# Kernel optimization log

Hardware: AMD Instinct MI355X
Metric: run time of the kernel (lower is better)

The kernel has to match this reference:

```python
import jax, jax.numpy as jnp
import numpy as np

N, E, H, C, F_IN = 10000, 160000, 8, 128, 4  # nodes, edges, heads, per-head dim, input feats
D = H * C  # 1024 concat dim


def _gelu(v):
    return jax.nn.gelu(v, approximate=False)  # torch F.gelu default is exact erf


def _gat(x, src, dst, w, a_s, a_d, b):
    """PyG GATConv (concat=True, negative_slope=0.2), self-loops already in src/dst."""
    n = x.shape[0]
    h = (x @ w).reshape(n, H, C)                      # [N,H,C]
    e = (h * a_s).sum(-1)[src] + (h * a_d).sum(-1)[dst]  # [E,H] per-edge logits
    e = jnp.where(e > 0, e, 0.2 * e)                  # LeakyReLU(0.2)
    m = jax.lax.stop_gradient(jax.ops.segment_max(e, dst, num_segments=n))
    p = jnp.exp(e - m[dst])
    z = jax.ops.segment_sum(p, dst, num_segments=n)   # [N,H]
    alpha = p / z[dst]                                # softmax over incoming edges
    out = jax.ops.segment_sum(h[src] * alpha[:, :, None], dst, num_segments=n)
    return out.reshape(n, D) + b


def setup_inputs() -> dict:
    key = jax.random.key(0)
    ks = jax.random.split(key, 24)
    s = 0.05
    inp = {
        "x": jax.random.normal(ks[0], (N, F_IN), dtype=jnp.float32),
        "edge_index": jax.random.randint(ks[1], (2, E), 0, N),
        "w1": jax.random.normal(ks[2], (F_IN, D)) * s,
        "asrc1": jax.random.normal(ks[3], (H, C)) * s,
        "adst1": jax.random.normal(ks[4], (H, C)) * s,
        "bias1": jnp.zeros((D,), jnp.float32),
        "w2": jax.random.normal(ks[5], (C, D)) * s,
        "asrc2": jax.random.normal(ks[6], (H, C)) * s,
        "adst2": jax.random.normal(ks[7], (H, C)) * s,
        "bias2": jnp.zeros((D,), jnp.float32),
        "w3": jax.random.normal(ks[8], (C, D)) * s,
        "asrc3": jax.random.normal(ks[9], (H, C)) * s,
        "adst3": jax.random.normal(ks[10], (H, C)) * s,
        "bias3": jnp.zeros((D,), jnp.float32),
        "rw1": jax.random.normal(ks[11], (D, C)) * s,
        "rb1": jnp.zeros((C,), jnp.float32),
        "rw2": jax.random.normal(ks[12], (D, C)) * s,
        "rb2": jnp.zeros((C,), jnp.float32),
        "lw": jax.random.normal(ks[13], (D, C)) * s,
        "lb": jnp.zeros((C,), jnp.float32),
    }
    return inp


def reference(x, edge_index, w1, asrc1, adst1, bias1, w2, asrc2, adst2, bias2,
              w3, asrc3, adst3, bias3, rw1, rb1, rw2, rb2, lw, lb):
    loops = jnp.arange(N, dtype=edge_index.dtype)
    src = jnp.concatenate([edge_index[0], loops])
    dst = jnp.concatenate([edge_index[1], loops])
    h = _gat(x, src, dst, w1, asrc1, adst1, bias1)            # [N, 1024]
    h = _gat(_gelu(h) @ rw1 + rb1, src, dst, w2, asrc2, adst2, bias2)
    h = _gat(_gelu(h) @ rw2 + rb2, src, dst, w3, asrc3, adst3, bias3)
    return _gelu(h) @ lw + lb                                 # [N, 128]
```

## Files before the change

### kernel.cpp

```cpp
#include <hip/hip_runtime.h>
#include <hip/hip_fp16.h>
#include <math.h>


#define THREADS 256
#define CAP 128

typedef _Float16 f16x8 __attribute__((ext_vector_type(8)));
typedef float f32x4 __attribute__((ext_vector_type(4)));

struct __align__(8) Half4 { __half2 a, b; };

__device__ __forceinline__ float gelu_exact(float x) {
  return 0.5f * x * (1.0f + erff(x * 0.70710678118654752f));
}


__global__ __launch_bounds__(256) void prep_kernel(
    const int* __restrict__ ei, int E, int ET, int* __restrict__ counts,
    const float* __restrict__ w2, const float* __restrict__ w3,
    const float* __restrict__ rw1, const float* __restrict__ rw2,
    const float* __restrict__ lw,
    __half* __restrict__ wt2, __half* __restrict__ wt3,
    __half* __restrict__ rwt1, __half* __restrict__ rwt2,
    __half* __restrict__ lwt,
    const float* __restrict__ w1,
    const float* __restrict__ as1, const float* __restrict__ ad1,
    const float* __restrict__ as2, const float* __restrict__ ad2,
    const float* __restrict__ as3, const float* __restrict__ ad3,
    float* __restrict__ ws1, float* __restrict__ wd1,
    float* __restrict__ ws2, float* __restrict__ wd2,
    float* __restrict__ ws3, float* __restrict__ wd3,
    int nHist) {
  __shared__ float tile[32][33];
  int bid = blockIdx.x;
  int t = threadIdx.x;

  if (bid < nHist) {
    int e = bid * 256 + t;
    if (e >= ET) return;
    int d = (e < E) ? ei[E + e] : (e - E);
    atomicAdd(&counts[d], 1);
    return;
  }
  bid -= nHist;
  if (bid < 640) {
    const float* in; __half* out; int K, Ncol;
    int z = bid >> 7, rem = bid & 127;
    switch (z) {
      case 0: in = w2;  out = wt2;  K = 128;  Ncol = 1024; break;
      case 1: in = w3;  out = wt3;  K = 128;  Ncol = 1024; break;
      case 2: in = rw1; out = rwt1; K = 1024; Ncol = 128;  break;
      case 3: in = rw2; out = rwt2; K = 1024; Ncol = 128;  break;
      default: in = lw; out = lwt;  K = 1024; Ncol = 128;  break;
    }
    int kt, ct;
    if (z < 2) { kt = rem >> 5; ct = rem & 31; }
    else       { kt = rem & 31; ct = rem >> 5; }
    int kb = kt * 32, cb = ct * 32;
    int tc = t & 31, tr = t >> 5;
#pragma unroll
    for (int r = tr; r < 32; r += 8)
      tile[r][tc] = in[(size_t)(kb + r) * Ncol + cb + tc];
    __syncthreads();
#pragma unroll
    for (int r = tr; r < 32; r += 8)
      out[(size_t)(cb + r) * K + kb + tc] = __float2half_rn(tile[tc][r]);
    return;
  }
  bid -= 640;
  {
    int h = bid & 7, yy = bid >> 3;
    int sel = t >> 7;
    int k = t & 127;
    const float* W; const float* av; float* outp; int K;
    switch (yy) {
      case 0: W = w2; av = sel ? ad2 : as2; outp = sel ? wd2 : ws2; K = 128; break;
      case 1: W = w3; av = sel ? ad3 : as3; outp = sel ? wd3 : ws3; K = 128; break;
      default: W = w1; av = sel ? ad1 : as1; outp = sel ? wd1 : ws1; K = 4; break;
    }
    if (k >= K) return;
    const float* wrow = W + (size_t)k * 1024 + h * 128;
    const float* arow = av + h * 128;
    float s = 0.f;
    for (int c = 0; c < 128; c += 4) {
      float4 wv = *(const float4*)&wrow[c];
      float4 a4 = *(const float4*)&arow[c];
      s += wv.x * a4.x + wv.y * a4.y + wv.z * a4.z + wv.w * a4.w;
    }
    outp[h * K + k] = s;
  }
}


__global__ __launch_bounds__(1024) void scan_scores_kernel(
    const int* __restrict__ counts, int* __restrict__ offsets,
    int* __restrict__ cursor, int n,
    const float* __restrict__ x,
    const float* __restrict__ ws1, const float* __restrict__ wd1,
    float* __restrict__ ssrc, float* __restrict__ sdst, int total) {
  __shared__ int sums[1024];
  if (blockIdx.x == 0) {
    int t = threadIdx.x;
    int per = (n + 1023) >> 10;
    int start = t * per; if (start > n) start = n;
    int end = start + per; if (end > n) end = n;
    int local = 0;
    for (int i = start; i < end; ++i) local += counts[i];
    sums[t] = local;
    __syncthreads();
    for (int off = 1; off < 1024; off <<= 1) {
      int add = (t >= off) ? sums[t - off] : 0;
      __syncthreads();
      sums[t] += add;
      __syncthreads();
    }
    int run = (t == 0) ? 0 : sums[t - 1];
    for (int i = start; i < end; ++i) {
      offsets[i] = run; cursor[i] = run; run += counts[i];
    }
    if (t == 1023) offsets[n] = run;
    return;
  }
  int idx = (blockIdx.x - 1) * 1024 + threadIdx.x;
  if (idx >= total) return;
  int nn = idx >> 3, h = idx & 7;
  float4 xv = *(const float4*)&x[nn * 4];
  float4 a = *(const float4*)&ws1[h * 4];
  float4 b = *(const float4*)&wd1[h * 4];
  ssrc[idx] = xv.x * a.x + xv.y * a.y + xv.z * a.z + xv.w * a.w;
  sdst[idx] = xv.x * b.x + xv.y * b.y + xv.z * b.z + xv.w * b.w;
}

__global__ void scatter_kernel(const int* __restrict__ ei, int E, int ET,
                               int* __restrict__ cursor, int* __restrict__ srcs) {
  int e = blockIdx.x * THREADS + threadIdx.x;
  if (e >= ET) return;
  int s = (e < E) ? ei[e] : (e - E);
  int d = (e < E) ? ei[E + e] : (e - E);
  int pos = atomicAdd(&cursor[d], 1);
  srcs[pos] = s;
}


__global__ __launch_bounds__(256) void attnagg_p(const __half* __restrict__ P16,
                                                 const int* __restrict__ srcs,
                                                 const int* __restrict__ offsets,
                                                 const float* __restrict__ ssrc,
                                                 const float* __restrict__ sdst,
                                                 __half* __restrict__ Y16, int NP) {
  __shared__ float lal[4][CAP][8];
  __shared__ int ls[4][CAP];
  __shared__ float szinv[4][8];
  int w = threadIdx.x >> 6, lane = threadIdx.x & 63;
  int n = blockIdx.x * 4 + w;
  int start = offsets[n], deg = offsets[n + 1] - start;
  int head = lane & 7, es = lane >> 3;
  float sd = sdst[n * 8 + head];
  int c2 = lane * 2;
  float accx[8] = {}, accy[8] = {};
  float s = 0.f;
  for (int cc = 0; cc < deg; cc += CAP) {
    int cm = min(CAP, deg - cc);
    for (int i = es; i < cm; i += 8) {
      int sp = srcs[start + cc + i];
      float v = ssrc[sp * 8 + head] + sd;
      v = (v > 0.f) ? v : 0.2f * v;
      float e = __expf(v);
      lal[w][i][head] = e;
      if (head == 0) ls[w][i] = sp;
      s += e;
    }
    int i = 0;
    for (; i + 1 < cm; i += 2) {
      int sp0 = ls[w][i], sp1 = ls[w][i + 1];
      float4 a00 = *(float4*)&lal[w][i][0];
      float4 a01 = *(float4*)&lal[w][i][4];
      float4 a10 = *(float4*)&lal[w][i + 1][0];
      float4 a11 = *(float4*)&lal[w][i + 1][4];
      float2 p0 = __half22float2(*(const __half2*)&P16[(size_t)sp0 * 128 + c2]);
      float2 p1 = __half22float2(*(const __half2*)&P16[(size_t)sp1 * 128 + c2]);
      float a0[8] = {a00.x, a00.y, a00.z, a00.w, a01.x, a01.y, a01.z, a01.w};
      float a1[8] = {a10.x, a10.y, a10.z, a10.w, a11.x, a11.y, a11.z, a11.w};
#pragma unroll
      for (int h = 0; h < 8; ++h) {
        accx[h] += a0[h] * p0.x; accy[h] += a0[h] * p0.y;
        accx[h] += a1[h] * p1.x; accy[h] += a1[h] * p1.y;
      }
    }
    if (i < cm) {
      int sp0 = ls[w][i];
      float4 a00 = *(float4*)&lal[w][i][0];
      float4 a01 = *(float4*)&lal[w][i][4];
      float2 p0 = __half22float2(*(const __half2*)&P16[(size_t)sp0 * 128 + c2]);
      float a0[8] = {a00.x, a00.y, a00.z, a00.w, a01.x, a01.y, a01.z, a01.w};
#pragma unroll
      for (int h = 0; h < 8; ++h) {
        accx[h] += a0[h] * p0.x; accy[h] += a0[h] * p0.y;
      }
    }
  }
#pragma unroll
  for (int mask = 8; mask <= 32; mask <<= 1)
    s += __shfl_xor(s, mask);
  if (es == 0) szinv[w][head] = 1.f / s;
#pragma unroll
  for (int h = 0; h < 8; ++h) {
    float zi = szinv[w][h];
    *(__half2*)&Y16[((size_t)h * NP + n) * 128 + c2] =
        __floats2half2_rn(accx[h] * zi, accy[h] * zi);
  }
}


__global__ __launch_bounds__(256) void attnagg_x(const float* __restrict__ x,
                                                 const int* __restrict__ srcs,
                                                 const int* __restrict__ offsets,
                                                 const float* __restrict__ ssrc,
                                                 const float* __restrict__ sdst,
                                                 float* __restrict__ Y1, int NP) {
  __shared__ float lal[4][CAP][8];
  __shared__ int ls[4][CAP];
  __shared__ float szinv[4][8];
  int w = threadIdx.x >> 6, lane = threadIdx.x & 63;
  int n = blockIdx.x * 4 + w;
  int start = offsets[n], deg = offsets[n + 1] - start;
  int head = lane & 7, es = lane >> 3;
  float sd = sdst[n * 8 + head];
  int eo = lane >> 5, hb = (lane >> 2) & 7, ch = lane & 3;
  float acc = 0.f;
  float s = 0.f;
  for (int cc = 0; cc < deg; cc += CAP) {
    int cm = min(CAP, deg - cc);
    for (int i = es; i < cm; i += 8) {
      int sp = srcs[start + cc + i];
      float v = ssrc[sp * 8 + head] + sd;
      v = (v > 0.f) ? v : 0.2f * v;
      float e = __expf(v);
      lal[w][i][head] = e;
      if (head == 0) ls[w][i] = sp;
      s += e;
    }
    for (int i = eo; i < cm; i += 2) {
      int sp = ls[w][i];
      float a = lal[w][i][hb];
      acc += a * x[sp * 4 + ch];
    }
  }
#pragma unroll
  for (int mask = 8; mask <= 32; mask <<= 1)
    s += __shfl_xor(s, mask);
  if (es == 0) szinv[w][head] = 1.f / s;
  acc += __shfl_xor(acc, 32);
  if (lane < 32) {
    float zi = szinv[w][hb];
    Y1[((size_t)hb * NP + n) * 4 + ch] = acc * zi;
  }
}


template <typename OutT, bool SC>
__global__ __launch_bounds__(512) void tail_mfma(const __half* __restrict__ Y16,
                                                 const __half* __restrict__ WtA,
                                                 const float* __restrict__ biasA,
                                                 const __half* __restrict__ WtP,
                                                 const float* __restrict__ biasP,
                                                 OutT* __restrict__ out, int N, int NP,
                                                 const float* __restrict__ wsn,
                                                 const float* __restrict__ wdn,
                                                 float* __restrict__ ssrc,
                                                 float* __restrict__ sdst) {
  __shared__ __half Gt[32][1032];
  __shared__ __half Pl[32][136];
  int w = threadIdx.x >> 6, lane = threadIdx.x & 63;
  int r0 = blockIdx.x * 32;
  int m = lane & 15, quad = lane >> 4;
  {
    int h = w;
    const __half* py0 = Y16 + ((size_t)h * NP + r0 + m) * 128 + quad * 8;
    const __half* py1 = py0 + (size_t)16 * 128;
    f16x8 bf0[4], bf1[4];
#pragma unroll
    for (int kk = 0; kk < 4; ++kk) {
      bf0[kk] = *(const f16x8*)(py0 + kk * 32);
      bf1[kk] = *(const f16x8*)(py1 + kk * 32);
    }
#pragma unroll
    for (int tile = 0; tile < 8; ++tile) {
      int gc = h * 128 + tile * 16;
      const __half* pa = WtA + (size_t)(gc + m) * 128 + quad * 8;
      f16x8 a[4];
#pragma unroll
      for (int kk = 0; kk < 4; ++kk) a[kk] = *(const f16x8*)(pa + kk * 32);
      f32x4 acc0 = {0.f, 0.f, 0.f, 0.f}, acc1 = {0.f, 0.f, 0.f, 0.f};
#pragma unroll
      for (int kk = 0; kk < 4; ++kk) {
        acc0 = __builtin_amdgcn_mfma_f32_16x16x32_f16(a[kk], bf0[kk], acc0, 0, 0, 0);
        acc1 = __builtin_amdgcn_mfma_f32_16x16x32_f16(a[kk], bf1[kk], acc1, 0, 0, 0);
      }
      float4 b4 = *(const float4*)&biasA[gc + quad * 4];
      Half4 p0, p1;
      p0.a = __floats2half2_rn(gelu_exact(acc0[0] + b4.x), gelu_exact(acc0[1] + b4.y));
      p0.b = __floats2half2_rn(gelu_exact(acc0[2] + b4.z), gelu_exact(acc0[3] + b4.w));
      p1.a = __floats2half2_rn(gelu_exact(acc1[0] + b4.x), gelu_exact(acc1[1] + b4.y));
      p1.b = __floats2half2_rn(gelu_exact(acc1[2] + b4.z), gelu_exact(acc1[3] + b4.w));
      *(Half4*)&Gt[m][gc + quad * 4] = p0;
      *(Half4*)&Gt[16 + m][gc + quad * 4] = p1;
    }
  }
  __syncthreads();
  {
    int c0 = w * 16;
    const __half* pa = WtP + (size_t)(c0 + m) * 1024 + quad * 8;
    f32x4 acc0 = {0.f, 0.f, 0.f, 0.f}, acc1 = {0.f, 0.f, 0.f, 0.f};
#pragma unroll 8
    for (int k = 0; k < 1024; k += 32) {
      f16x8 a = *(const f16x8*)(pa + k);
      f16x8 b0 = *(const f16x8*)&Gt[m][quad * 8 + k];
      f16x8 b1 = *(const f16x8*)&Gt[16 + m][quad * 8 + k];
      acc0 = __builtin_amdgcn_mfma_f32_16x16x32_f16(a, b0, acc0, 0, 0, 0);
      acc1 = __builtin_amdgcn_mfma_f32_16x16x32_f16(a, b1, acc1, 0, 0, 0);
    }
    float4 b4 = *(const float4*)&biasP[c0 + quad * 4];
    int row0 = r0 + m, row1 = r0 + 16 + m;
    if constexpr (__is_same(OutT, __half)) {
      Half4 p, q;
      p.a = __floats2half2_rn(acc0[0] + b4.x, acc0[1] + b4.y);
      p.b = __floats2half2_rn(acc0[2] + b4.z, acc0[3] + b4.w);
      q.a = __floats2half2_rn(acc1[0] + b4.x, acc1[1] + b4.y);
      q.b = __floats2half2_rn(acc1[2] + b4.z, acc1[3] + b4.w);
      if constexpr (SC) {
        *(Half4*)&Pl[m][c0 + quad * 4] = p;
        *(Half4*)&Pl[16 + m][c0 + quad * 4] = q;
      }
      if (row0 < N) *(Half4*)&out[(size_t)row0 * 128 + c0 + quad * 4] = p;
      if (row1 < N) *(Half4*)&out[(size_t)row1 * 128 + c0 + quad * 4] = q;
    } else {
      if (row0 < N)
        *(float4*)&out[(size_t)row0 * 128 + c0 + quad * 4] =
            make_float4(acc0[0] + b4.x, acc0[1] + b4.y, acc0[2] + b4.z, acc0[3] + b4.w);
      if (row1 < N)
        *(float4*)&out[(size_t)row1 * 128 + c0 + quad * 4] =
            make_float4(acc1[0] + b4.x, acc1[1] + b4.y, acc1[2] + b4.z, acc1[3] + b4.w);
    }
  }
  if constexpr (SC) {
    __syncthreads();
    int head = lane & 7, es = lane >> 3;
    const float* wsp = wsn + head * 128 + es * 16;
    const float* wdp = wdn + head * 128 + es * 16;
    float wsr[16], wdr[16];
#pragma unroll
    for (int j = 0; j < 16; ++j) { wsr[j] = wsp[j]; wdr[j] = wdp[j]; }
#pragma unroll
    for (int r = 0; r < 4; ++r) {
      int row = w * 4 + r;
      f16x8 p0 = *(const f16x8*)&Pl[row][es * 16];
      f16x8 p1 = *(const f16x8*)&Pl[row][es * 16 + 8];
      float s1 = 0.f, s2 = 0.f;
#pragma unroll
      for (int j = 0; j < 8; ++j) {
        float v = (float)p0[j];
        s1 += v * wsr[j]; s2 += v * wdr[j];
      }
#pragma unroll
      for (int j = 0; j < 8; ++j) {
        float v = (float)p1[j];
        s1 += v * wsr[8 + j]; s2 += v * wdr[8 + j];
      }
#pragma unroll
      for (int mask = 8; mask <= 32; mask <<= 1) {
        s1 += __shfl_xor(s1, mask);
        s2 += __shfl_xor(s2, mask);
      }
      int nn = r0 + row;
      if (es == 0 && nn < N) { ssrc[nn * 8 + head] = s1; sdst[nn * 8 + head] = s2; }
    }
  }
}


template <typename OutT, bool SC>
__global__ __launch_bounds__(512) void tail1_kernel(const float* __restrict__ Y1,
                                                    const float* __restrict__ w,
                                                    const float* __restrict__ biasA,
                                                    const __half* __restrict__ WtP,
                                                    const float* __restrict__ biasP,
                                                    OutT* __restrict__ out, int N, int NP,
                                                    const float* __restrict__ wsn,
                                                    const float* __restrict__ wdn,
                                                    float* __restrict__ ssrc,
                                                    float* __restrict__ sdst) {
  __shared__ __half Gt[32][1032];
  __shared__ __half Pl[32][136];
  int t = threadIdx.x;
  int r0 = blockIdx.x * 32;
  {
    int c0 = (t & 255) * 4;
    int h = c0 >> 7;
    float4 wa = *(const float4*)&w[c0];
    float4 wb = *(const float4*)&w[1024 + c0];
    float4 wc = *(const float4*)&w[2048 + c0];
    float4 wd = *(const float4*)&w[3072 + c0];
    float4 b4 = *(const float4*)&biasA[c0];
#pragma unroll 4
    for (int r = t >> 8; r < 32; r += 2) {
      float4 yv = *(const float4*)&Y1[((size_t)h * NP + r0 + r) * 4];
      float o0 = gelu_exact(yv.x * wa.x + yv.y * wb.x + yv.z * wc.x + yv.w * wd.x + b4.x);
      float o1 = gelu_exact(yv.x * wa.y + yv.y * wb.y + yv.z * wc.y + yv.w * wd.y + b4.y);
      float o2 = gelu_exact(yv.x * wa.z + yv.y * wb.z + yv.z * wc.z + yv.w * wd.z + b4.z);
      float o3 = gelu_exact(yv.x * wa.w + yv.y * wb.w + yv.z * wc.w + yv.w * wd.w + b4.w);
      Half4 p;
      p.a = __floats2half2_rn(o0, o1);
      p.b = __floats2half2_rn(o2, o3);
      *(Half4*)&Gt[r][c0] = p;
    }
  }
  __syncthreads();
  int wv = t >> 6, lane = t & 63;
  int m = lane & 15, quad = lane >> 4;
  {
    int c0 = wv * 16;
    const __half* pa = WtP + (size_t)(c0 + m) * 1024 + quad * 8;
    f32x4 acc0 = {0.f, 0.f, 0.f, 0.f}, acc1 = {0.f, 0.f, 0.f, 0.f};
#pragma unroll 8
    for (int k = 0; k < 1024; k += 32) {
      f16x8 a = *(const f16x8*)(pa + k);
      f16x8 b0 = *(const f16x8*)&Gt[m][quad * 8 + k];
      f16x8 b1 = *(const f16x8*)&Gt[16 + m][quad * 8 + k];
      acc0 = __builtin_amdgcn_mfma_f32_16x16x32_f16(a, b0, acc0, 0, 0, 0);
      acc1 = __builtin_amdgcn_mfma_f32_16x16x32_f16(a, b1, acc1, 0, 0, 0);
    }
    float4 b4 = *(const float4*)&biasP[c0 + quad * 4];
    int row0 = r0 + m, row1 = r0 + 16 + m;
    if constexpr (__is_same(OutT, __half)) {
      Half4 p, q;
      p.a = __floats2half2_rn(acc0[0] + b4.x, acc0[1] + b4.y);
      p.b = __floats2half2_rn(acc0[2] + b4.z, acc0[3] + b4.w);
      q.a = __floats2half2_rn(acc1[0] + b4.x, acc1[1] + b4.y);
      q.b = __floats2half2_rn(acc1[2] + b4.z, acc1[3] + b4.w);
      if constexpr (SC) {
        *(Half4*)&Pl[m][c0 + quad * 4] = p;
        *(Half4*)&Pl[16 + m][c0 + quad * 4] = q;
      }
      if (row0 < N) *(Half4*)&out[(size_t)row0 * 128 + c0 + quad * 4] = p;
      if (row1 < N) *(Half4*)&out[(size_t)row1 * 128 + c0 + quad * 4] = q;
    } else {
      if (row0 < N)
        *(float4*)&out[(size_t)row0 * 128 + c0 + quad * 4] =
            make_float4(acc0[0] + b4.x, acc0[1] + b4.y, acc0[2] + b4.z, acc0[3] + b4.w);
      if (row1 < N)
        *(float4*)&out[(size_t)row1 * 128 + c0 + quad * 4] =
            make_float4(acc1[0] + b4.x, acc1[1] + b4.y, acc1[2] + b4.z, acc1[3] + b4.w);
    }
  }
  if constexpr (SC) {
    __syncthreads();
    int head = lane & 7, es = lane >> 3;
    const float* wsp = wsn + head * 128 + es * 16;
    const float* wdp = wdn + head * 128 + es * 16;
    float wsr[16], wdr[16];
#pragma unroll
    for (int j = 0; j < 16; ++j) { wsr[j] = wsp[j]; wdr[j] = wdp[j]; }
#pragma unroll
    for (int r = 0; r < 4; ++r) {
      int row = wv * 4 + r;
      f16x8 p0 = *(const f16x8*)&Pl[row][es * 16];
      f16x8 p1 = *(const f16x8*)&Pl[row][es * 16 + 8];
      float s1 = 0.f, s2 = 0.f;
#pragma unroll
      for (int j = 0; j < 8; ++j) {
        float v = (float)p0[j];
        s1 += v * wsr[j]; s2 += v * wdr[j];
      }
#pragma unroll
      for (int j = 0; j < 8; ++j) {
        float v = (float)p1[j];
        s1 += v * wsr[8 + j]; s2 += v * wdr[8 + j];
      }
#pragma unroll
      for (int mask = 8; mask <= 32; mask <<= 1) {
        s1 += __shfl_xor(s1, mask);
        s2 += __shfl_xor(s2, mask);
      }
      int nn = r0 + row;
      if (es == 0 && nn < N) { ssrc[nn * 8 + head] = s1; sdst[nn * 8 + head] = s2; }
    }
  }
}


extern "C" void kernel_launch(void* const* d_in, const int* in_sizes, int n_in,
                              void* d_out, int out_size, void* d_ws, size_t ws_size,
                              hipStream_t stream) {
  const float* x   = (const float*)d_in[0];
  const int*   ei  = (const int*)d_in[1];
  const float* w1  = (const float*)d_in[2];
  const float* as1 = (const float*)d_in[3];
  const float* ad1 = (const float*)d_in[4];
  const float* b1  = (const float*)d_in[5];
  const float* w2  = (const float*)d_in[6];
  const float* as2 = (const float*)d_in[7];
  const float* ad2 = (const float*)d_in[8];
  const float* b2  = (const float*)d_in[9];
  const float* w3  = (const float*)d_in[10];
  const float* as3 = (const float*)d_in[11];
  const float* ad3 = (const float*)d_in[12];
  const float* b3  = (const float*)d_in[13];
  const float* rw1 = (const float*)d_in[14];
  const float* rb1 = (const float*)d_in[15];
  const float* rw2 = (const float*)d_in[16];
  const float* rb2 = (const float*)d_in[17];
  const float* lw  = (const float*)d_in[18];
  const float* lb  = (const float*)d_in[19];

  int N = in_sizes[0] / 4;
  int E = in_sizes[1] / 2;
  int ET = E + N;
  int nRow32 = (N + 31) / 32;
  int NP = nRow32 * 32;
  (void)ws_size;

  char* wsb = (char*)d_ws;
  size_t off = 0;
  auto alloc = [&](size_t bytes) -> void* {
    void* p = wsb + off;
    off += (bytes + 255) & ~(size_t)255;
    return p;
  };
  __half* P16  = (__half*)alloc((size_t)N * 128 * 2);
  __half* Y16  = (__half*)alloc((size_t)8 * NP * 128 * 2);
  float*  Y1   = (float*)alloc((size_t)8 * NP * 4 * 4);
  __half* wt2  = (__half*)alloc((size_t)1024 * 128 * 2);
  __half* wt3  = (__half*)alloc((size_t)1024 * 128 * 2);
  __half* rwt1 = (__half*)alloc((size_t)128 * 1024 * 2);
  __half* rwt2 = (__half*)alloc((size_t)128 * 1024 * 2);
  __half* lwt  = (__half*)alloc((size_t)128 * 1024 * 2);
  float* ws1 = (float*)alloc(8 * 4 * 4);
  float* wd1 = (float*)alloc(8 * 4 * 4);
  float* ws2 = (float*)alloc(8 * 128 * 4);
  float* wd2 = (float*)alloc(8 * 128 * 4);
  float* ws3 = (float*)alloc(8 * 128 * 4);
  float* wd3 = (float*)alloc(8 * 128 * 4);
  float* ssrc   = (float*)alloc((size_t)N * 8 * 4);
  float* sdst   = (float*)alloc((size_t)N * 8 * 4);
  int* counts  = (int*)alloc((size_t)N * 4);
  int* offsets = (int*)alloc((size_t)(N + 1) * 4);
  int* cursor  = (int*)alloc((size_t)N * 4);
  int* srcs    = (int*)alloc((size_t)ET * 4);

  dim3 blk(THREADS);
  dim3 blk512(512);

  int nHist = (ET + THREADS - 1) / THREADS;

  hipMemsetAsync(counts, 0, (size_t)N * 4, stream);

  prep_kernel<<<dim3(nHist + 640 + 24), blk, 0, stream>>>(
      ei, E, ET, counts,
      w2, w3, rw1, rw2, lw, wt2, wt3, rwt1, rwt2, lwt,
      w1, as1, ad1, as2, ad2, as3, ad3,
      ws1, wd1, ws2, wd2, ws3, wd3, nHist);

  int total1 = N * 8;
  int nSc = (total1 + 1023) / 1024;
  scan_scores_kernel<<<dim3(1 + nSc), dim3(1024), 0, stream>>>(
      counts, offsets, cursor, N, x, ws1, wd1, ssrc, sdst, total1);

  scatter_kernel<<<dim3(nHist), blk, 0, stream>>>(ei, E, ET, cursor, srcs);

  dim3 gNode4(N / 4);
  dim3 gRow32(nRow32);

  attnagg_x<<<gNode4, blk, 0, stream>>>(x, srcs, offsets, ssrc, sdst, Y1, NP);
  tail1_kernel<__half, true><<<gRow32, blk512, 0, stream>>>(
      Y1, w1, b1, rwt1, rb1, P16, N, NP, ws2, wd2, ssrc, sdst);

  attnagg_p<<<gNode4, blk, 0, stream>>>(P16, srcs, offsets, ssrc, sdst, Y16, NP);
  tail_mfma<__half, true><<<gRow32, blk512, 0, stream>>>(
      Y16, wt2, b2, rwt2, rb2, P16, N, NP, ws3, wd3, ssrc, sdst);

  attnagg_p<<<gNode4, blk, 0, stream>>>(P16, srcs, offsets, ssrc, sdst, Y16, NP);
  tail_mfma<float, false><<<gRow32, blk512, 0, stream>>>(
      Y16, wt3, b3, lwt, lb, (float*)d_out, N, NP, nullptr, nullptr, nullptr, nullptr);
}
```

Before: 287.9 us.

## Fuse attention aggregation into per-layer MFMA tail kernels via shared memory

Merges each layer's edge aggregation kernel into the following dense MFMA kernel. Each 512-thread block aggregates its 32 rows straight into LDS instead of writing the 8-head Y16/Y1 intermediates to global memory and reading them back. This drops three launches and the global round trip of the large intermediate. The node features and attention scores are now double-buffered so that a fused kernel never overwrites the buffers its neighbours still read. In exchange, there are fewer blocks (32 rows each instead of 4 nodes), the gather phase has less parallelism, and the larger LDS footprint may lower occupancy.

```diff
diff --git a/kernel.cpp b/kernel.cpp
--- a/kernel.cpp
+++ b/kernel.cpp
@@ -4,7 +4,6 @@
 
 
 #define THREADS 256
-#define CAP 128
 
 typedef _Float16 f16x8 __attribute__((ext_vector_type(8)));
 typedef float f32x4 __attribute__((ext_vector_type(4)));
@@ -143,259 +142,62 @@
 }
 
 
-__global__ __launch_bounds__(256) void attnagg_p(const __half* __restrict__ P16,
-                                                 const int* __restrict__ srcs,
-                                                 const int* __restrict__ offsets,
-                                                 const float* __restrict__ ssrc,
-                                                 const float* __restrict__ sdst,
-                                                 __half* __restrict__ Y16, int NP) {
-  __shared__ float lal[4][CAP][8];
-  __shared__ int ls[4][CAP];
-  __shared__ float szinv[4][8];
-  int w = threadIdx.x >> 6, lane = threadIdx.x & 63;
-  int n = blockIdx.x * 4 + w;
-  int start = offsets[n], deg = offsets[n + 1] - start;
+__global__ __launch_bounds__(512) void layer1_kernel(
+    const float* __restrict__ x,
+    const int* __restrict__ srcs, const int* __restrict__ offsets,
+    const float* __restrict__ ssrc, const float* __restrict__ sdst,
+    const float* __restrict__ w, const float* __restrict__ biasA,
+    const __half* __restrict__ WtP, const float* __restrict__ biasP,
+    __half* __restrict__ out, int N,
+    const float* __restrict__ wsn, const float* __restrict__ wdn,
+    float* __restrict__ ssrc_n, float* __restrict__ sdst_n) {
+  __shared__ __half Gt[32][1032];
+  __shared__ float Y1l[32][36];
+  __shared__ __align__(16) char scratch[9216];
+  __shared__ float szinv[8][8];
+  float (*lsc)[32][8] = reinterpret_cast<float(*)[32][8]>(scratch);
+  int (*lsi)[32] = reinterpret_cast<int(*)[32]>(scratch + 8192);
+  __half (*Pl)[136] = reinterpret_cast<__half(*)[136]>(scratch);
+
+  int wv = threadIdx.x >> 6, lane = threadIdx.x & 63;
+  int r0 = blockIdx.x * 32;
   int head = lane & 7, es = lane >> 3;
-  float sd = sdst[n * 8 + head];
-  int c2 = lane * 2;
-  float accx[8] = {}, accy[8] = {};
-  float s = 0.f;
-  for (int cc = 0; cc < deg; cc += CAP) {
-    int cm = min(CAP, deg - cc);
-    for (int i = es; i < cm; i += 8) {
-      int sp = srcs[start + cc + i];
-      float v = ssrc[sp * 8 + head] + sd;
-      v = (v > 0.f) ? v : 0.2f * v;
-      float e = __expf(v);
-      lal[w][i][head] = e;
-      if (head == 0) ls[w][i] = sp;
-      s += e;
-    }
-    int i = 0;
-    for (; i + 1 < cm; i += 2) {
-      int sp0 = ls[w][i], sp1 = ls[w][i + 1];
-      float4 a00 = *(float4*)&lal[w][i][0];
-      float4 a01 = *(float4*)&lal[w][i][4];
-      float4 a10 = *(float4*)&lal[w][i + 1][0];
-      float4 a11 = *(float4*)&lal[w][i + 1][4];
-      float2 p0 = __half22float2(*(const __half2*)&P16[(size_t)sp0 * 128 + c2]);
-      float2 p1 = __half22float2(*(const __half2*)&P16[(size_t)sp1 * 128 + c2]);
-      float a0[8] = {a00.x, a00.y, a00.z, a00.w, a01.x, a01.y, a01.z, a01.w};
-      float a1[8] = {a10.x, a10.y, a10.z, a10.w, a11.x, a11.y, a11.z, a11.w};
-#pragma unroll
-      for (int h = 0; h < 8; ++h) {
-        accx[h] += a0[h] * p0.x; accy[h] += a0[h] * p0.y;
-        accx[h] += a1[h] * p1.x; accy[h] += a1[h] * p1.y;
-      }
-    }
-    if (i < cm) {
-      int sp0 = ls[w][i];
-      float4 a00 = *(float4*)&lal[w][i][0];
-      float4 a01 = *(float4*)&lal[w][i][4];
-      float2 p0 = __half22float2(*(const __half2*)&P16[(size_t)sp0 * 128 + c2]);
-      float a0[8] = {a00.x, a00.y, a00.z, a00.w, a01.x, a01.y, a01.z, a01.w};
-#pragma unroll
-      for (int h = 0; h < 8; ++h) {
-        accx[h] += a0[h] * p0.x; accy[h] += a0[h] * p0.y;
-      }
-    }
-  }
-#pragma unroll
-  for (int mask = 8; mask <= 32; mask <<= 1)
-    s += __shfl_xor(s, mask);
-  if (es == 0) szinv[w][head] = 1.f / s;
-#pragma unroll
-  for (int h = 0; h < 8; ++h) {
-    float zi = szinv[w][h];
-    *(__half2*)&Y16[((size_t)h * NP + n) * 128 + c2] =
-        __floats2half2_rn(accx[h] * zi, accy[h] * zi);
-  }
-}
-
-
-__global__ __launch_bounds__(256) void attnagg_x(const float* __restrict__ x,
-                                                 const int* __restrict__ srcs,
-                                                 const int* __restrict__ offsets,
-                                                 const float* __restrict__ ssrc,
-                                                 const float* __restrict__ sdst,
-                                                 float* __restrict__ Y1, int NP) {
-  __shared__ float lal[4][CAP][8];
-  __shared__ int ls[4][CAP];
-  __shared__ float szinv[4][8];
-  int w = threadIdx.x >> 6, lane = threadIdx.x & 63;
-  int n = blockIdx.x * 4 + w;
-  int start = offsets[n], deg = offsets[n + 1] - start;
-  int head = lane & 7, es = lane >> 3;
-  float sd = sdst[n * 8 + head];
   int eo = lane >> 5, hb = (lane >> 2) & 7, ch = lane & 3;
-  float acc = 0.f;
-  float s = 0.f;
-  for (int cc = 0; cc < deg; cc += CAP) {
-    int cm = min(CAP, deg - cc);
-    for (int i = es; i < cm; i += 8) {
-      int sp = srcs[start + cc + i];
-      float v = ssrc[sp * 8 + head] + sd;
-      v = (v > 0.f) ? v : 0.2f * v;
-      float e = __expf(v);
-      lal[w][i][head] = e;
-      if (head == 0) ls[w][i] = sp;
-      s += e;
-    }
-    for (int i = eo; i < cm; i += 2) {
-      int sp = ls[w][i];
-      float a = lal[w][i][hb];
-      acc += a * x[sp * 4 + ch];
-    }
-  }
-#pragma unroll
-  for (int mask = 8; mask <= 32; mask <<= 1)
-    s += __shfl_xor(s, mask);
-  if (es == 0) szinv[w][head] = 1.f / s;
-  acc += __shfl_xor(acc, 32);
-  if (lane < 32) {
-    float zi = szinv[w][hb];
-    Y1[((size_t)hb * NP + n) * 4 + ch] = acc * zi;
-  }
-}
-
-
-template <typename OutT, bool SC>
-__global__ __launch_bounds__(512) void tail_mfma(const __half* __restrict__ Y16,
-                                                 const __half* __restrict__ WtA,
-                                                 const float* __restrict__ biasA,
-                                                 const __half* __restrict__ WtP,
-                                                 const float* __restrict__ biasP,
-                                                 OutT* __restrict__ out, int N, int NP,
-                                                 const float* __restrict__ wsn,
-                                                 const float* __restrict__ wdn,
-                                                 float* __restrict__ ssrc,
-                                                 float* __restrict__ sdst) {
-  __shared__ __half Gt[32][1032];
-  __shared__ __half Pl[32][136];
-  int w = threadIdx.x >> 6, lane = threadIdx.x & 63;
-  int r0 = blockIdx.x * 32;
-  int m = lane & 15, quad = lane >> 4;
-  {
-    int h = w;
-    const __half* py0 = Y16 + ((size_t)h * NP + r0 + m) * 128 + quad * 8;
-    const __half* py1 = py0 + (size_t)16 * 128;
-    f16x8 bf0[4], bf1[4];
-#pragma unroll
-    for (int kk = 0; kk < 4; ++kk) {
-      bf0[kk] = *(const f16x8*)(py0 + kk * 32);
-      bf1[kk] = *(const f16x8*)(py1 + kk * 32);
-    }
-#pragma unroll
-    for (int tile = 0; tile < 8; ++tile) {
-      int gc = h * 128 + tile * 16;
-      const __half* pa = WtA + (size_t)(gc + m) * 128 + quad * 8;
-      f16x8 a[4];
-#pragma unroll
-      for (int kk = 0; kk < 4; ++kk) a[kk] = *(const f16x8*)(pa + kk * 32);
-      f32x4 acc0 = {0.f, 0.f, 0.f, 0.f}, acc1 = {0.f, 0.f, 0.f, 0.f};
-#pragma unroll
-      for (int kk = 0; kk < 4; ++kk) {
-        acc0 = __builtin_amdgcn_mfma_f32_16x16x32_f16(a[kk], bf0[kk], acc0, 0, 0, 0);
-        acc1 = __builtin_amdgcn_mfma_f32_16x16x32_f16(a[kk], bf1[kk], acc1, 0, 0, 0);
-      }
-      float4 b4 = *(const float4*)&biasA[gc + quad * 4];
-      Half4 p0, p1;
-      p0.a = __floats2half2_rn(gelu_exact(acc0[0] + b4.x), gelu_exact(acc0[1] + b4.y));
-      p0.b = __floats2half2_rn(gelu_exact(acc0[2] + b4.z), gelu_exact(acc0[3] + b4.w));
-      p1.a = __floats2half2_rn(gelu_exact(acc1[0] + b4.x), gelu_exact(acc1[1] + b4.y));
-      p1.b = __floats2half2_rn(gelu_exact(acc1[2] + b4.z), gelu_exact(acc1[3] + b4.w));
-      *(Half4*)&Gt[m][gc + quad * 4] = p0;
-      *(Half4*)&Gt[16 + m][gc + quad * 4] = p1;
-    }
+
+  for (int j = 0; j < 4; ++j) {
+    int row = wv * 4 + j, n = r0 + row;
+    if (n >= N) {
+      if (lane < 32) Y1l[row][hb * 4 + ch] = 0.f;
+      continue;
+    }
+    int start = offsets[n], deg = offsets[n + 1] - start;
+    float sd = sdst[n * 8 + head];
+    float acc = 0.f, s = 0.f;
+    for (int cc = 0; cc < deg; cc += 32) {
+      int cm = min(32, deg - cc);
+      for (int i = es; i < cm; i += 8) {
+        int sp = srcs[start + cc + i];
+        float v = ssrc[sp * 8 + head] + sd;
+        v = (v > 0.f) ? v : 0.2f * v;
+        float e = __expf(v);
+        lsc[wv][i][head] = e;
+        if (head == 0) lsi[wv][i] = sp;
+        s += e;
+      }
+      for (int i = eo; i < cm; i += 2) {
+        int sp = lsi[wv][i];
+        acc += lsc[wv][i][hb] * x[sp * 4 + ch];
+      }
+    }
+#pragma unroll
+    for (int mask = 8; mask <= 32; mask <<= 1) s += __shfl_xor(s, mask);
+    if (es == 0) szinv[wv][head] = 1.f / s;
+    acc += __shfl_xor(acc, 32);
+    if (lane < 32) Y1l[row][hb * 4 + ch] = acc * szinv[wv][hb];
   }
   __syncthreads();
   {
-    int c0 = w * 16;
-    const __half* pa = WtP + (size_t)(c0 + m) * 1024 + quad * 8;
-    f32x4 acc0 = {0.f, 0.f, 0.f, 0.f}, acc1 = {0.f, 0.f, 0.f, 0.f};
-#pragma unroll 8
-    for (int k = 0; k < 1024; k += 32) {
-      f16x8 a = *(const f16x8*)(pa + k);
-      f16x8 b0 = *(const f16x8*)&Gt[m][quad * 8 + k];
-      f16x8 b1 = *(const f16x8*)&Gt[16 + m][quad * 8 + k];
-      acc0 = __builtin_amdgcn_mfma_f32_16x16x32_f16(a, b0, acc0, 0, 0, 0);
-      acc1 = __builtin_amdgcn_mfma_f32_16x16x32_f16(a, b1, acc1, 0, 0, 0);
-    }
-    float4 b4 = *(const float4*)&biasP[c0 + quad * 4];
-    int row0 = r0 + m, row1 = r0 + 16 + m;
-    if constexpr (__is_same(OutT, __half)) {
-      Half4 p, q;
-      p.a = __floats2half2_rn(acc0[0] + b4.x, acc0[1] + b4.y);
-      p.b = __floats2half2_rn(acc0[2] + b4.z, acc0[3] + b4.w);
-      q.a = __floats2half2_rn(acc1[0] + b4.x, acc1[1] + b4.y);
-      q.b = __floats2half2_rn(acc1[2] + b4.z, acc1[3] + b4.w);
-      if constexpr (SC) {
-        *(Half4*)&Pl[m][c0 + quad * 4] = p;
-        *(Half4*)&Pl[16 + m][c0 + quad * 4] = q;
-      }
-      if (row0 < N) *(Half4*)&out[(size_t)row0 * 128 + c0 + quad * 4] = p;
-      if (row1 < N) *(Half4*)&out[(size_t)row1 * 128 + c0 + quad * 4] = q;
-    } else {
-      if (row0 < N)
-        *(float4*)&out[(size_t)row0 * 128 + c0 + quad * 4] =
-            make_float4(acc0[0] + b4.x, acc0[1] + b4.y, acc0[2] + b4.z, acc0[3] + b4.w);
-      if (row1 < N)
-        *(float4*)&out[(size_t)row1 * 128 + c0 + quad * 4] =
-            make_float4(acc1[0] + b4.x, acc1[1] + b4.y, acc1[2] + b4.z, acc1[3] + b4.w);
-    }
-  }
-  if constexpr (SC) {
-    __syncthreads();
-    int head = lane & 7, es = lane >> 3;
-    const float* wsp = wsn + head * 128 + es * 16;
-    const float* wdp = wdn + head * 128 + es * 16;
-    float wsr[16], wdr[16];
-#pragma unroll
-    for (int j = 0; j < 16; ++j) { wsr[j] = wsp[j]; wdr[j] = wdp[j]; }
-#pragma unroll
-    for (int r = 0; r < 4; ++r) {
-      int row = w * 4 + r;
-      f16x8 p0 = *(const f16x8*)&Pl[row][es * 16];
-      f16x8 p1 = *(const f16x8*)&Pl[row][es * 16 + 8];
-      float s1 = 0.f, s2 = 0.f;
-#pragma unroll
-      for (int j = 0; j < 8; ++j) {
-        float v = (float)p0[j];
-        s1 += v * wsr[j]; s2 += v * wdr[j];
-      }
-#pragma unroll
-      for (int j = 0; j < 8; ++j) {
-        float v = (float)p1[j];
-        s1 += v * wsr[8 + j]; s2 += v * wdr[8 + j];
-      }
-#pragma unroll
-      for (int mask = 8; mask <= 32; mask <<= 1) {
-        s1 += __shfl_xor(s1, mask);
-        s2 += __shfl_xor(s2, mask);
-      }
-      int nn = r0 + row;
-      if (es == 0 && nn < N) { ssrc[nn * 8 + head] = s1; sdst[nn * 8 + head] = s2; }
-    }
-  }
-}
-
-
-template <typename OutT, bool SC>
-__global__ __launch_bounds__(512) void tail1_kernel(const float* __restrict__ Y1,
-                                                    const float* __restrict__ w,
-                                                    const float* __restrict__ biasA,
-                                                    const __half* __restrict__ WtP,
-                                                    const float* __restrict__ biasP,
-                                                    OutT* __restrict__ out, int N, int NP,
-                                                    const float* __restrict__ wsn,
-                                                    const float* __restrict__ wdn,
-                                                    float* __restrict__ ssrc,
-                                                    float* __restrict__ sdst) {
-  __shared__ __half Gt[32][1032];
-  __shared__ __half Pl[32][136];
-  int t = threadIdx.x;
-  int r0 = blockIdx.x * 32;
-  {
+    int t = threadIdx.x;
     int c0 = (t & 255) * 4;
     int h = c0 >> 7;
     float4 wa = *(const float4*)&w[c0];
@@ -405,7 +207,7 @@
     float4 b4 = *(const float4*)&biasA[c0];
 #pragma unroll 4
     for (int r = t >> 8; r < 32; r += 2) {
-      float4 yv = *(const float4*)&Y1[((size_t)h * NP + r0 + r) * 4];
+      float4 yv = *(const float4*)&Y1l[r][h * 4];
       float o0 = gelu_exact(yv.x * wa.x + yv.y * wb.x + yv.z * wc.x + yv.w * wd.x + b4.x);
       float o1 = gelu_exact(yv.x * wa.y + yv.y * wb.y + yv.z * wc.y + yv.w * wd.y + b4.y);
       float o2 = gelu_exact(yv.x * wa.z + yv.y * wb.z + yv.z * wc.z + yv.w * wd.z + b4.z);
@@ -417,7 +219,6 @@
     }
   }
   __syncthreads();
-  int wv = t >> 6, lane = t & 63;
   int m = lane & 15, quad = lane >> 4;
   {
     int c0 = wv * 16;
@@ -433,6 +234,183 @@
     }
     float4 b4 = *(const float4*)&biasP[c0 + quad * 4];
     int row0 = r0 + m, row1 = r0 + 16 + m;
+    Half4 p, q;
+    p.a = __floats2half2_rn(acc0[0] + b4.x, acc0[1] + b4.y);
+    p.b = __floats2half2_rn(acc0[2] + b4.z, acc0[3] + b4.w);
+    q.a = __floats2half2_rn(acc1[0] + b4.x, acc1[1] + b4.y);
+    q.b = __floats2half2_rn(acc1[2] + b4.z, acc1[3] + b4.w);
+    *(Half4*)&Pl[m][c0 + quad * 4] = p;
+    *(Half4*)&Pl[16 + m][c0 + quad * 4] = q;
+    if (row0 < N) *(Half4*)&out[(size_t)row0 * 128 + c0 + quad * 4] = p;
+    if (row1 < N) *(Half4*)&out[(size_t)row1 * 128 + c0 + quad * 4] = q;
+  }
+  __syncthreads();
+  {
+    const float* wsp = wsn + head * 128 + es * 16;
+    const float* wdp = wdn + head * 128 + es * 16;
+    float wsr[16], wdr[16];
+#pragma unroll
+    for (int j = 0; j < 16; ++j) { wsr[j] = wsp[j]; wdr[j] = wdp[j]; }
+#pragma unroll
+    for (int r = 0; r < 4; ++r) {
+      int row = wv * 4 + r;
+      f16x8 p0 = *(const f16x8*)&Pl[row][es * 16];
+      f16x8 p1 = *(const f16x8*)&Pl[row][es * 16 + 8];
+      float s1 = 0.f, s2 = 0.f;
+#pragma unroll
+      for (int j = 0; j < 8; ++j) {
+        float v = (float)p0[j];
+        s1 += v * wsr[j]; s2 += v * wdr[j];
+      }
+#pragma unroll
+      for (int j = 0; j < 8; ++j) {
+        float v = (float)p1[j];
+        s1 += v * wsr[8 + j]; s2 += v * wdr[8 + j];
+      }
+#pragma unroll
+      for (int mask = 8; mask <= 32; mask <<= 1) {
+        s1 += __shfl_xor(s1, mask);
+        s2 += __shfl_xor(s2, mask);
+      }
+      int nn = r0 + row;
+      if (es == 0 && nn < N) { ssrc_n[nn * 8 + head] = s1; sdst_n[nn * 8 + head] = s2; }
+    }
+  }
+}
+
+
+template <typename OutT, bool SC>
+__global__ __launch_bounds__(512) void layer_p_kernel(
+    const __half* __restrict__ P16,
+    const int* __restrict__ srcs, const int* __restrict__ offsets,
+    const float* __restrict__ ssrc, const float* __restrict__ sdst,
+    const __half* __restrict__ WtA, const float* __restrict__ biasA,
+    const __half* __restrict__ WtP, const float* __restrict__ biasP,
+    OutT* __restrict__ out, int N,
+    const float* __restrict__ wsn, const float* __restrict__ wdn,
+    float* __restrict__ ssrc_n, float* __restrict__ sdst_n) {
+  __shared__ __half Yl[32][1032];
+  __shared__ __align__(16) char scratch[9216];
+  __shared__ float szinv[8][8];
+  float (*lsc)[32][8] = reinterpret_cast<float(*)[32][8]>(scratch);
+  int (*lsi)[32] = reinterpret_cast<int(*)[32]>(scratch + 8192);
+  __half (*Pl)[136] = reinterpret_cast<__half(*)[136]>(scratch);
+
+  int w = threadIdx.x >> 6, lane = threadIdx.x & 63;
+  int r0 = blockIdx.x * 32;
+  int head = lane & 7, es = lane >> 3;
+  int c2 = lane * 2;
+  int m = lane & 15, quad = lane >> 4;
+
+  for (int j = 0; j < 4; ++j) {
+    int row = w * 4 + j, n = r0 + row;
+    if (n >= N) {
+      __half2 z = __floats2half2_rn(0.f, 0.f);
+#pragma unroll
+      for (int h = 0; h < 8; ++h) *(__half2*)&Yl[row][h * 128 + c2] = z;
+      continue;
+    }
+    int start = offsets[n], deg = offsets[n + 1] - start;
+    float sd = sdst[n * 8 + head];
+    float accx[8] = {}, accy[8] = {};
+    float s = 0.f;
+    for (int cc = 0; cc < deg; cc += 32) {
+      int cm = min(32, deg - cc);
+      for (int i = es; i < cm; i += 8) {
+        int sp = srcs[start + cc + i];
+        float v = ssrc[sp * 8 + head] + sd;
+        v = (v > 0.f) ? v : 0.2f * v;
+        float e = __expf(v);
+        lsc[w][i][head] = e;
+        if (head == 0) lsi[w][i] = sp;
+        s += e;
+      }
+      int i = 0;
+      for (; i + 1 < cm; i += 2) {
+        int sp0 = lsi[w][i], sp1 = lsi[w][i + 1];
+        float4 a00 = *(float4*)&lsc[w][i][0];
+        float4 a01 = *(float4*)&lsc[w][i][4];
+        float4 a10 = *(float4*)&lsc[w][i + 1][0];
+        float4 a11 = *(float4*)&lsc[w][i + 1][4];
+        float2 p0 = __half22float2(*(const __half2*)&P16[(size_t)sp0 * 128 + c2]);
+        float2 p1 = __half22float2(*(const __half2*)&P16[(size_t)sp1 * 128 + c2]);
+        float a0[8] = {a00.x, a00.y, a00.z, a00.w, a01.x, a01.y, a01.z, a01.w};
+        float a1[8] = {a10.x, a10.y, a10.z, a10.w, a11.x, a11.y, a11.z, a11.w};
+#pragma unroll
+        for (int h = 0; h < 8; ++h) {
+          accx[h] += a0[h] * p0.x; accy[h] += a0[h] * p0.y;
+          accx[h] += a1[h] * p1.x; accy[h] += a1[h] * p1.y;
+        }
+      }
+      if (i < cm) {
+        int sp0 = lsi[w][i];
+        float4 a00 = *(float4*)&lsc[w][i][0];
+        float4 a01 = *(float4*)&lsc[w][i][4];
+        float2 p0 = __half22float2(*(const __half2*)&P16[(size_t)sp0 * 128 + c2]);
+        float a0[8] = {a00.x, a00.y, a00.z, a00.w, a01.x, a01.y, a01.z, a01.w};
+#pragma unroll
+        for (int h = 0; h < 8; ++h) {
+          accx[h] += a0[h] * p0.x; accy[h] += a0[h] * p0.y;
+        }
+      }
+    }
+#pragma unroll
+    for (int mask = 8; mask <= 32; mask <<= 1) s += __shfl_xor(s, mask);
+    if (es == 0) szinv[w][head] = 1.f / s;
+#pragma unroll
+    for (int h = 0; h < 8; ++h) {
+      float zi = szinv[w][h];
+      *(__half2*)&Yl[row][h * 128 + c2] =
+          __floats2half2_rn(accx[h] * zi, accy[h] * zi);
+    }
+  }
+  __syncthreads();
+  {
+    int h = w;
+    f16x8 bf0[4], bf1[4];
+#pragma unroll
+    for (int kk = 0; kk < 4; ++kk) {
+      bf0[kk] = *(const f16x8*)&Yl[m][h * 128 + quad * 8 + kk * 32];
+      bf1[kk] = *(const f16x8*)&Yl[16 + m][h * 128 + quad * 8 + kk * 32];
+    }
+#pragma unroll
+    for (int tile = 0; tile < 8; ++tile) {
+      int gc = h * 128 + tile * 16;
+      const __half* pa = WtA + (size_t)(gc + m) * 128 + quad * 8;
+      f16x8 a[4];
+#pragma unroll
+      for (int kk = 0; kk < 4; ++kk) a[kk] = *(const f16x8*)(pa + kk * 32);
+      f32x4 acc0 = {0.f, 0.f, 0.f, 0.f}, acc1 = {0.f, 0.f, 0.f, 0.f};
+#pragma unroll
+      for (int kk = 0; kk < 4; ++kk) {
+        acc0 = __builtin_amdgcn_mfma_f32_16x16x32_f16(a[kk], bf0[kk], acc0, 0, 0, 0);
+        acc1 = __builtin_amdgcn_mfma_f32_16x16x32_f16(a[kk], bf1[kk], acc1, 0, 0, 0);
+      }
+      float4 b4 = *(const float4*)&biasA[gc + quad * 4];
+      Half4 p0, p1;
+      p0.a = __floats2half2_rn(gelu_exact(acc0[0] + b4.x), gelu_exact(acc0[1] + b4.y));
+      p0.b = __floats2half2_rn(gelu_exact(acc0[2] + b4.z), gelu_exact(acc0[3] + b4.w));
+      p1.a = __floats2half2_rn(gelu_exact(acc1[0] + b4.x), gelu_exact(acc1[1] + b4.y));
+      p1.b = __floats2half2_rn(gelu_exact(acc1[2] + b4.z), gelu_exact(acc1[3] + b4.w));
+      *(Half4*)&Yl[m][gc + quad * 4] = p0;
+      *(Half4*)&Yl[16 + m][gc + quad * 4] = p1;
+    }
+  }
+  __syncthreads();
+  {
+    int c0 = w * 16;
+    const __half* pa = WtP + (size_t)(c0 + m) * 1024 + quad * 8;
+    f32x4 acc0 = {0.f, 0.f, 0.f, 0.f}, acc1 = {0.f, 0.f, 0.f, 0.f};
+#pragma unroll 8
+    for (int k = 0; k < 1024; k += 32) {
+      f16x8 a = *(const f16x8*)(pa + k);
+      f16x8 b0 = *(const f16x8*)&Yl[m][quad * 8 + k];
+      f16x8 b1 = *(const f16x8*)&Yl[16 + m][quad * 8 + k];
+      acc0 = __builtin_amdgcn_mfma_f32_16x16x32_f16(a, b0, acc0, 0, 0, 0);
+      acc1 = __builtin_amdgcn_mfma_f32_16x16x32_f16(a, b1, acc1, 0, 0, 0);
+    }
+    float4 b4 = *(const float4*)&biasP[c0 + quad * 4];
+    int row0 = r0 + m, row1 = r0 + 16 + m;
     if constexpr (__is_same(OutT, __half)) {
       Half4 p, q;
       p.a = __floats2half2_rn(acc0[0] + b4.x, acc0[1] + b4.y);
@@ -456,7 +434,6 @@
   }
   if constexpr (SC) {
     __syncthreads();
-    int head = lane & 7, es = lane >> 3;
     const float* wsp = wsn + head * 128 + es * 16;
     const float* wdp = wdn + head * 128 + es * 16;
     float wsr[16], wdr[16];
@@ -464,7 +441,7 @@
     for (int j = 0; j < 16; ++j) { wsr[j] = wsp[j]; wdr[j] = wdp[j]; }
 #pragma unroll
     for (int r = 0; r < 4; ++r) {
-      int row = wv * 4 + r;
+      int row = w * 4 + r;
       f16x8 p0 = *(const f16x8*)&Pl[row][es * 16];
       f16x8 p1 = *(const f16x8*)&Pl[row][es * 16 + 8];
       float s1 = 0.f, s2 = 0.f;
@@ -484,7 +461,7 @@
         s2 += __shfl_xor(s2, mask);
       }
       int nn = r0 + row;
-      if (es == 0 && nn < N) { ssrc[nn * 8 + head] = s1; sdst[nn * 8 + head] = s2; }
+      if (es == 0 && nn < N) { ssrc_n[nn * 8 + head] = s1; sdst_n[nn * 8 + head] = s2; }
     }
   }
 }
@@ -518,7 +495,6 @@
   int E = in_sizes[1] / 2;
   int ET = E + N;
   int nRow32 = (N + 31) / 32;
-  int NP = nRow32 * 32;
   (void)ws_size;
 
   char* wsb = (char*)d_ws;
@@ -528,9 +504,8 @@
     off += (bytes + 255) & ~(size_t)255;
     return p;
   };
-  __half* P16  = (__half*)alloc((size_t)N * 128 * 2);
-  __half* Y16  = (__half*)alloc((size_t)8 * NP * 128 * 2);
-  float*  Y1   = (float*)alloc((size_t)8 * NP * 4 * 4);
+  __half* P16a = (__half*)alloc((size_t)N * 128 * 2);
+  __half* P16b = (__half*)alloc((size_t)N * 128 * 2);
   __half* wt2  = (__half*)alloc((size_t)1024 * 128 * 2);
   __half* wt3  = (__half*)alloc((size_t)1024 * 128 * 2);
   __half* rwt1 = (__half*)alloc((size_t)128 * 1024 * 2);
@@ -542,8 +517,10 @@
   float* wd2 = (float*)alloc(8 * 128 * 4);
   float* ws3 = (float*)alloc(8 * 128 * 4);
   float* wd3 = (float*)alloc(8 * 128 * 4);
-  float* ssrc   = (float*)alloc((size_t)N * 8 * 4);
-  float* sdst   = (float*)alloc((size_t)N * 8 * 4);
+  float* ssrcA = (float*)alloc((size_t)N * 8 * 4);
+  float* sdstA = (float*)alloc((size_t)N * 8 * 4);
+  float* ssrcB = (float*)alloc((size_t)N * 8 * 4);
+  float* sdstB = (float*)alloc((size_t)N * 8 * 4);
   int* counts  = (int*)alloc((size_t)N * 4);
   int* offsets = (int*)alloc((size_t)(N + 1) * 4);
   int* cursor  = (int*)alloc((size_t)N * 4);
@@ -551,7 +528,6 @@
 
   dim3 blk(THREADS);
   dim3 blk512(512);
-
   int nHist = (ET + THREADS - 1) / THREADS;
 
   hipMemsetAsync(counts, 0, (size_t)N * 4, stream);
@@ -565,22 +541,21 @@
   int total1 = N * 8;
   int nSc = (total1 + 1023) / 1024;
   scan_scores_kernel<<<dim3(1 + nSc), dim3(1024), 0, stream>>>(
-      counts, offsets, cursor, N, x, ws1, wd1, ssrc, sdst, total1);
+      counts, offsets, cursor, N, x, ws1, wd1, ssrcA, sdstA, total1);
 
   scatter_kernel<<<dim3(nHist), blk, 0, stream>>>(ei, E, ET, cursor, srcs);
 
-  dim3 gNode4(N / 4);
   dim3 gRow32(nRow32);
 
-  attnagg_x<<<gNode4, blk, 0, stream>>>(x, srcs, offsets, ssrc, sdst, Y1, NP);
-  tail1_kernel<__half, true><<<gRow32, blk512, 0, stream>>>(
-      Y1, w1, b1, rwt1, rb1, P16, N, NP, ws2, wd2, ssrc, sdst);
-
-  attnagg_p<<<gNode4, blk, 0, stream>>>(P16, srcs, offsets, ssrc, sdst, Y16, NP);
-  tail_mfma<__half, true><<<gRow32, blk512, 0, stream>>>(
-      Y16, wt2, b2, rwt2, rb2, P16, N, NP, ws3, wd3, ssrc, sdst);
-
-  attnagg_p<<<gNode4, blk, 0, stream>>>(P16, srcs, offsets, ssrc, sdst, Y16, NP);
-  tail_mfma<float, false><<<gRow32, blk512, 0, stream>>>(
-      Y16, wt3, b3, lwt, lb, (float*)d_out, N, NP, nullptr, nullptr, nullptr, nullptr);
-}
+  layer1_kernel<<<gRow32, blk512, 0, stream>>>(
+      x, srcs, offsets, ssrcA, sdstA, w1, b1, rwt1, rb1, P16a, N,
+      ws2, wd2, ssrcB, sdstB);
+
+  layer_p_kernel<__half, true><<<gRow32, blk512, 0, stream>>>(
+      P16a, srcs, offsets, ssrcB, sdstB, wt2, b2, rwt2, rb2, P16b, N,
+      ws3, wd3, ssrcA, sdstA);
+
+  layer_p_kernel<float, false><<<gRow32, blk512, 0, stream>>>(
+      P16b, srcs, offsets, ssrcA, sdstA, wt3, b3, lwt, lb, (float*)d_out, N,
+      nullptr, nullptr, nullptr, nullptr);
+}
```

Measured after the change: 289.7 us. Within noise of the previous version (+0.6%).
